# Performance work log

Hardware: AMD Instinct MI355X
Metric: run time of the kernel (lower is better)

## Reference

```python
import jax, jax.numpy as jnp
import numpy as np

N = 100000   # num nodes
E = 1200000  # num edges
D = 64       # feature dim (input and both hidden layers)
R = 4        # num relations


def setup_inputs() -> dict:
    key = jax.random.key(0)
    ks = jax.random.split(key, 16)

    def p(k, shape, scale=0.05):
        return jax.random.normal(k, shape, dtype=jnp.float32) * scale

    inp = {
        "x": p(ks[0], (N, D), 1.0),
        "src": jax.random.randint(ks[1], (E,), 0, N),
        "dst": jax.random.randint(ks[2], (E,), 0, N),
        "rel": jax.random.randint(ks[3], (E,), 0, R),
    }
    i = 4
    for layer in (1, 2):
        inp[f"conv{layer}_w"] = p(ks[i], (D, R * D)); i += 1
        inp[f"conv{layer}_b"] = jnp.zeros((D,), jnp.float32)
        inp[f"conv{layer}_ws"] = p(ks[i], (D, D)); i += 1
        inp[f"conv{layer}_bs"] = jnp.zeros((D,), jnp.float32)
        inp[f"hw{layer}_pw"] = p(ks[i], (D, 2 * D)); i += 1
        inp[f"hw{layer}_pb"] = jnp.zeros((D,), jnp.float32)
        inp[f"hw{layer}_tw"] = p(ks[i], (D, 2 * D)); i += 1
        inp[f"hw{layer}_tb"] = jnp.full((D,), -2.0, jnp.float32)  # transform bias init -2
    return inp


def _rgc(x, src, dst, rel, w, b, ws, bs):
    # RelationalGraphConv: per-(node, relation) scatter-mean of source features,
    # then linear over concatenated relation slots + self-loop linear + sigmoid.
    msg = x[src]                                  # [E, D] gather
    seg = dst * R + rel                           # [E] flattened (node, relation) id
    s = jax.ops.segment_sum(msg, seg, num_segments=N * R)          # [N*R, D]
    cnt = jax.ops.segment_sum(jnp.ones((msg.shape[0], 1), msg.dtype), seg,
                              num_segments=N * R)                  # [N*R, 1]
    upd = (s / jnp.maximum(cnt, 1.0)).reshape(N, R * x.shape[1])   # [N, R*D]
    out = upd @ w.T + b + x @ ws.T + bs
    return jax.nn.sigmoid(out)


def _highway(h, prev, pw, pb, tw, tb):
    c = jnp.concatenate([h, prev], axis=1)        # [N, 2D]
    pr = jax.nn.relu(c @ pw.T + pb)
    g = jax.nn.sigmoid(c @ tw.T + tb)
    return g * pr + (1.0 - g) * h


def reference(x, src, dst, rel,
              conv1_w, conv1_b, conv1_ws, conv1_bs,
              hw1_pw, hw1_pb, hw1_tw, hw1_tb,
              conv2_w, conv2_b, conv2_ws, conv2_bs,
              hw2_pw, hw2_pb, hw2_tw, hw2_tb):
    h1 = _rgc(x, src, dst, rel, conv1_w, conv1_b, conv1_ws, conv1_bs)
    g1 = _highway(h1, x, hw1_pw, hw1_pb, hw1_tw, hw1_tb)   # prev_gcn = input
    h2 = _rgc(g1, src, dst, rel, conv2_w, conv2_b, conv2_ws, conv2_bs)
    g2 = _highway(h2, h1, hw2_pw, hw2_pb, hw2_tw, hw2_tb)  # prev_gcn = h1 (conv1 output)
    return g2  # node_feature, [N, D]
```

## Files before the change

### kernel.cpp

```cpp
#include <hip/hip_runtime.h>

#define NN 100000
#define NE 1200000
#define NRR 400000
#define NBIN 98
#define SSZ2 384

typedef float f32x4 __attribute__((ext_vector_type(4)));
typedef __bf16 bf16x8 __attribute__((ext_vector_type(8)));

__device__ __forceinline__ float sigmoidf_(float x){ return 1.0f/(1.0f+__expf(-x)); }

__global__ __launch_bounds__(256)
void binhist_kernel(const int* __restrict__ dst, const int* __restrict__ rel,
                    int* __restrict__ bincnt){
  __shared__ int h[NBIN];
  int t = threadIdx.x;
  if (t < NBIN) h[t] = 0;
  __syncthreads();
  for (int e = blockIdx.x*256 + t; e < NE; e += 64*256){
    int bin = (dst[e]*4 + rel[e]) >> 12;
    atomicAdd(&h[bin], 1);
  }
  __syncthreads();
  if (t < NBIN && h[t]) atomicAdd(&bincnt[t], h[t]);
}

__global__ void binscan_kernel(const int* __restrict__ bincnt, int* __restrict__ binoff,
                               int* __restrict__ bincur, int* __restrict__ soff){
  if (threadIdx.x == 0){
    int s = 0;
    for (int i = 0; i < NBIN; ++i){ binoff[i] = s; bincur[i] = s; s += bincnt[i]; }
    binoff[NBIN] = NE;
    soff[NRR] = NE;
  }
}

__global__ __launch_bounds__(256)
void passA_kernel(const int* __restrict__ src, const int* __restrict__ dst,
                  const int* __restrict__ rel, int* __restrict__ bincur,
                  unsigned* __restrict__ ebin){
  __shared__ int h[NBIN], runbase[NBIN];
  int t = threadIdx.x;
  if (t < NBIN) h[t] = 0;
  __syncthreads();
  int lo = blockIdx.x*8192, hi = min(lo + 8192, NE);
  for (int e = lo + t; e < hi; e += 256)
    atomicAdd(&h[(dst[e]*4 + rel[e]) >> 12], 1);
  __syncthreads();
  if (t < NBIN){
    runbase[t] = h[t] ? atomicAdd(&bincur[t], h[t]) : 0;
    h[t] = 0;
  }
  __syncthreads();
  for (int e = lo + t; e < hi; e += 256){
    int seg = dst[e]*4 + rel[e];
    int bin = seg >> 12;
    int p = runbase[bin] + atomicAdd(&h[bin], 1);
    ebin[p] = (unsigned)src[e] | ((unsigned)(seg & 4095) << 17);
  }
}

__global__ __launch_bounds__(1024)
void passB_kernel(const unsigned* __restrict__ ebin, const int* __restrict__ binoff,
                  int* __restrict__ soff, unsigned* __restrict__ ebuck){
  __shared__ int st[4096];
  __shared__ int wsum[16], wbase[16];
  const int bin = blockIdx.x;
  const int t = threadIdx.x;
  const int base = binoff[bin], end = binoff[bin+1];
  #pragma unroll
  for (int i = 0; i < 4; ++i) st[t*4 + i] = 0;
  __syncthreads();
  for (int e = base + t; e < end; e += 1024)
    atomicAdd(&st[(ebin[e] >> 17) & 4095], 1);
  __syncthreads();
  int h0 = st[t*4], h1 = st[t*4+1], h2 = st[t*4+2], h3 = st[t*4+3];
  int lsum = h0 + h1 + h2 + h3;
  int lane = t & 63, wv = t >> 6;
  int inc = lsum;
  #pragma unroll
  for (int o = 1; o < 64; o <<= 1){ int u = __shfl_up(inc, o); if (lane >= o) inc += u; }
  if (lane == 63) wsum[wv] = inc;
  __syncthreads();
  if (t == 0){ int s = 0; for (int i = 0; i < 16; ++i){ wbase[i] = s; s += wsum[i]; } }
  __syncthreads();
  int ex = base + wbase[wv] + (inc - lsum);
  int s0 = ex, s1 = ex + h0, s2 = s1 + h1, s3 = s2 + h2;
  st[t*4] = s0; st[t*4+1] = s1; st[t*4+2] = s2; st[t*4+3] = s3;
  int sg = bin*4096 + t*4;
  if (sg   < NRR) soff[sg]   = s0;
  if (sg+1 < NRR) soff[sg+1] = s1;
  if (sg+2 < NRR) soff[sg+2] = s2;
  if (sg+3 < NRR) soff[sg+3] = s3;
  __syncthreads();
  for (int e = base + t; e < end; e += 1024){
    unsigned u = ebin[e];
    int p = atomicAdd(&st[(u >> 17) & 4095], 1);
    ebuck[p] = u & 0x1FFFFu;
  }
}

__global__ void tobf16_kernel(const float* __restrict__ xf, __bf16* __restrict__ xb){
  int i = (blockIdx.x*256 + threadIdx.x)*8;
  if (i < NN*64){
    f32x4 a = *(const f32x4*)(xf + i);
    f32x4 b = *(const f32x4*)(xf + i + 4);
    bf16x8 r;
    r[0]=(__bf16)a[0]; r[1]=(__bf16)a[1]; r[2]=(__bf16)a[2]; r[3]=(__bf16)a[3];
    r[4]=(__bf16)b[0]; r[5]=(__bf16)b[1]; r[6]=(__bf16)b[2]; r[7]=(__bf16)b[3];
    *(bf16x8*)(xb + i) = r;
  }
}

__global__ void prep_kernel(const float* __restrict__ w,  const float* __restrict__ b,
                            const float* __restrict__ ws, const float* __restrict__ bs,
                            const float* __restrict__ pw, const float* __restrict__ pb,
                            const float* __restrict__ tw, const float* __restrict__ tb,
                            __bf16* __restrict__ W1, __bf16* __restrict__ W2,
                            float* __restrict__ bias1, float* __restrict__ bias2){
  int i = blockIdx.x*256 + threadIdx.x;
  if (i < 64*320) {
    int e = i & 7, lane = (i >> 3) & 63, j = (i >> 9) & 3, kbi = i >> 11;
    int n = j*16 + (lane & 15);
    int k = kbi*32 + (lane >> 4)*8 + e;
    float v = (k < 256) ? w[n*256 + k] : ws[n*64 + (k - 256)];
    W1[i] = (__bf16)v;
  }
  if (i < 128*128) {
    int e = i & 7, lane = (i >> 3) & 63, j = (i >> 9) & 7, kbi = i >> 12;
    int n = j*16 + (lane & 15);
    int k = kbi*32 + (lane >> 4)*8 + e;
    float v = (n < 64) ? pw[n*128 + k] : tw[(n - 64)*128 + k];
    W2[i] = (__bf16)v;
  }
  if (i < 64)  bias1[i] = b[i] + bs[i];
  if (i < 128) bias2[i] = (i < 64) ? pb[i] : tb[i-64];
}

__global__ __launch_bounds__(256)
void gather_kernel(const unsigned* __restrict__ ebuck, const int* __restrict__ soff,
                   const __bf16* __restrict__ inb, __bf16* __restrict__ segb){
  __shared__ int sof[33];
  __shared__ int ssrc[SSZ2];
  const int b = blockIdx.x;
  const int t = threadIdx.x;
  if (t < 33) sof[t] = soff[b*32 + t];
  __syncthreads();
  const int e0 = sof[0], e1 = sof[32];
  for (int e = e0 + t; e < e1; e += 256){
    int o = e - e0;
    if (o < SSZ2) ssrc[o] = (int)ebuck[e];
  }
  __syncthreads();

  const int fl = t & 7;
  const int g  = t >> 3;
  int o0 = sof[g] - e0;
  int c  = sof[g+1] - sof[g];
  if (o0 + c > SSZ2) c = max(0, SSZ2 - o0);

  f32x4 a0 = {0.f,0.f,0.f,0.f}, a1 = {0.f,0.f,0.f,0.f};
  f32x4 b0 = {0.f,0.f,0.f,0.f}, b1 = {0.f,0.f,0.f,0.f};
  int i = 0;
  for (; i + 2 <= c; i += 2){
    int s0 = ssrc[o0+i], s1 = ssrc[o0+i+1];
    bf16x8 v0 = *(const bf16x8*)(&inb[(size_t)s0*64 + fl*8]);
    bf16x8 v1 = *(const bf16x8*)(&inb[(size_t)s1*64 + fl*8]);
    a0[0]+=(float)v0[0]; a0[1]+=(float)v0[1]; a0[2]+=(float)v0[2]; a0[3]+=(float)v0[3];
    a1[0]+=(float)v0[4]; a1[1]+=(float)v0[5]; a1[2]+=(float)v0[6]; a1[3]+=(float)v0[7];
    b0[0]+=(float)v1[0]; b0[1]+=(float)v1[1]; b0[2]+=(float)v1[2]; b0[3]+=(float)v1[3];
    b1[0]+=(float)v1[4]; b1[1]+=(float)v1[5]; b1[2]+=(float)v1[6]; b1[3]+=(float)v1[7];
  }
  if (i < c){
    int s0 = ssrc[o0+i];
    bf16x8 v0 = *(const bf16x8*)(&inb[(size_t)s0*64 + fl*8]);
    a0[0]+=(float)v0[0]; a0[1]+=(float)v0[1]; a0[2]+=(float)v0[2]; a0[3]+=(float)v0[3];
    a1[0]+=(float)v0[4]; a1[1]+=(float)v0[5]; a1[2]+=(float)v0[6]; a1[3]+=(float)v0[7];
  }
  float inv = 1.0f / fmaxf((float)c, 1.0f);
  bf16x8 r;
  r[0]=(__bf16)((a0[0]+b0[0])*inv); r[1]=(__bf16)((a0[1]+b0[1])*inv);
  r[2]=(__bf16)((a0[2]+b0[2])*inv); r[3]=(__bf16)((a0[3]+b0[3])*inv);
  r[4]=(__bf16)((a1[0]+b1[0])*inv); r[5]=(__bf16)((a1[1]+b1[1])*inv);
  r[6]=(__bf16)((a1[2]+b1[2])*inv); r[7]=(__bf16)((a1[3]+b1[3])*inv);

  const int sgg = b*32 + g;
  const int n   = sgg >> 2, rr = sgg & 3;
  const int nb  = n >> 4,  ml = n & 15;
  const int kbi = rr*2 + (fl >> 2);
  const int kgs = fl & 3;
  *(bf16x8*)(&segb[(size_t)((nb*8 + kbi)*64 + kgs*16 + ml)*8]) = r;
}

#define HSP 72

template<bool LAYER1>
__global__ __launch_bounds__(256, 4)
void dense_kernel(const __bf16* __restrict__ segbs,
                  const __bf16* __restrict__ xinb,
                  const __bf16* __restrict__ prevb,
                  const __bf16* __restrict__ W1s,
                  const __bf16* __restrict__ W2s,
                  const float* __restrict__ bias1,
                  const float* __restrict__ bias2,
                  __bf16* __restrict__ hb,
                  __bf16* __restrict__ gb,
                  float* __restrict__ outp)
{
  __shared__ __align__(16) __bf16 hs[64*HSP];
  __shared__ __align__(16) float outs[64*64];

  const int tid  = threadIdx.x;
  const int lane = tid & 63;
  const int wv   = tid >> 6;
  const int mloc = lane & 15;
  const int kg   = lane >> 4;
  const int wb   = blockIdx.x*64 + wv*16;
  const int arow = min(wb + mloc, NN-1);
  const int nbq  = min(wb, NN-16) >> 4;
  const size_t abase = (size_t)nbq * (8*512);

  f32x4 acc1[4] = {};

  #pragma unroll
  for (int kbi = 0; kbi < 8; ++kbi) {
    bf16x8 af = *(const bf16x8*)(&segbs[abase + (size_t)(kbi*64 + lane)*8]);
    #pragma unroll
    for (int j = 0; j < 4; ++j) {
      bf16x8 bf = *(const bf16x8*)(&W1s[((kbi*4 + j)*64 + lane)*8]);
      acc1[j] = __builtin_amdgcn_mfma_f32_16x16x32_bf16(af, bf, acc1[j], 0,0,0);
    }
  }
  #pragma unroll
  for (int kb = 0; kb < 64; kb += 32) {
    bf16x8 af = *(const bf16x8*)(&xinb[(size_t)arow*64 + kb + kg*8]);
    const int kbi = 8 + (kb >> 5);
    #pragma unroll
    for (int j = 0; j < 4; ++j) {
      bf16x8 bf = *(const bf16x8*)(&W1s[((kbi*4 + j)*64 + lane)*8]);
      acc1[j] = __builtin_amdgcn_mfma_f32_16x16x32_bf16(af, bf, acc1[j], 0,0,0);
    }
  }

  #pragma unroll
  for (int j = 0; j < 4; ++j) {
    int col = j*16 + mloc;
    float b1 = bias1[col];
    #pragma unroll
    for (int r = 0; r < 4; ++r) {
      float hv = sigmoidf_(acc1[j][r] + b1);
      acc1[j][r] = hv;
      hs[(wv*16 + kg*4 + r)*HSP + col] = (__bf16)hv;
    }
  }

  if (LAYER1) {
    #pragma unroll
    for (int i = 0; i < 2; ++i) {
      int r2 = i*8 + (lane >> 3);
      int c2 = lane & 7;
      bf16x8 v = *(const bf16x8*)(&hs[(wv*16 + r2)*HSP + c2*8]);
      int grow = wb + r2;
      if (grow < NN) *(bf16x8*)(&hb[(size_t)grow*64 + c2*8]) = v;
    }
  }

  f32x4 acc2[8] = {};
  #pragma unroll
  for (int kb = 0; kb < 64; kb += 32) {
    bf16x8 af = *(const bf16x8*)(&hs[(wv*16 + mloc)*HSP + kb + kg*8]);
    const int kbi = kb >> 5;
    #pragma unroll
    for (int j = 0; j < 8; ++j) {
      bf16x8 bf = *(const bf16x8*)(&W2s[((kbi*8 + j)*64 + lane)*8]);
      acc2[j] = __builtin_amdgcn_mfma_f32_16x16x32_bf16(af, bf, acc2[j], 0,0,0);
    }
  }
  #pragma unroll
  for (int kb = 0; kb < 64; kb += 32) {
    bf16x8 af = *(const bf16x8*)(&prevb[(size_t)arow*64 + kb + kg*8]);
    const int kbi = 2 + (kb >> 5);
    #pragma unroll
    for (int j = 0; j < 8; ++j) {
      bf16x8 bf = *(const bf16x8*)(&W2s[((kbi*8 + j)*64 + lane)*8]);
      acc2[j] = __builtin_amdgcn_mfma_f32_16x16x32_bf16(af, bf, acc2[j], 0,0,0);
    }
  }

  #pragma unroll
  for (int j = 0; j < 4; ++j) {
    int col = j*16 + mloc;
    float bp = bias2[col];
    float bt = bias2[64 + col];
    #pragma unroll
    for (int r = 0; r < 4; ++r) {
      float pr = fmaxf(acc2[j][r] + bp, 0.0f);
      float g  = sigmoidf_(acc2[j+4][r] + bt);
      float hv = acc1[j][r];
      float ov = g*pr + (1.0f - g)*hv;
      if (LAYER1) {
        hs[(wv*16 + kg*4 + r)*HSP + col] = (__bf16)ov;
      } else {
        outs[(wv*16 + kg*4 + r)*64 + col] = ov;
      }
    }
  }
  if (LAYER1) {
    #pragma unroll
    for (int i = 0; i < 2; ++i) {
      int r2 = i*8 + (lane >> 3);
      int c2 = lane & 7;
      bf16x8 v = *(const bf16x8*)(&hs[(wv*16 + r2)*HSP + c2*8]);
      int grow = wb + r2;
      if (grow < NN) *(bf16x8*)(&gb[(size_t)grow*64 + c2*8]) = v;
    }
  } else {
    #pragma unroll
    for (int i = 0; i < 4; ++i) {
      int pos = i*256 + lane*4;
      int r2 = pos >> 6, c2 = pos & 63;
      int grow = wb + r2;
      if (grow < NN)
        *(f32x4*)(&outp[(size_t)grow*64 + c2]) =
            *(const f32x4*)(&outs[(wv*16 + r2)*64 + c2]);
    }
  }
}

extern "C" void kernel_launch(void* const* d_in, const int* in_sizes, int n_in,
                              void* d_out, int out_size, void* d_ws, size_t ws_size,
                              hipStream_t stream){
  const float* x    = (const float*)d_in[0];
  const int*   src  = (const int*)d_in[1];
  const int*   dst  = (const int*)d_in[2];
  const int*   rel  = (const int*)d_in[3];
  const float* c1w  = (const float*)d_in[4];
  const float* c1b  = (const float*)d_in[5];
  const float* c1ws = (const float*)d_in[6];
  const float* c1bs = (const float*)d_in[7];
  const float* h1pw = (const float*)d_in[8];
  const float* h1pb = (const float*)d_in[9];
  const float* h1tw = (const float*)d_in[10];
  const float* h1tb = (const float*)d_in[11];
  const float* c2w  = (const float*)d_in[12];
  const float* c2b  = (const float*)d_in[13];
  const float* c2ws = (const float*)d_in[14];
  const float* c2bs = (const float*)d_in[15];
  const float* h2pw = (const float*)d_in[16];
  const float* h2pb = (const float*)d_in[17];
  const float* h2tw = (const float*)d_in[18];
  const float* h2tb = (const float*)d_in[19];

  char* p = (char*)d_ws;
  __bf16* segb = (__bf16*)p;  p += (size_t)NRR*64*2;
  __bf16* xb   = (__bf16*)p;  p += (size_t)NN*64*2;
  __bf16* h1b  = (__bf16*)p;  p += (size_t)NN*64*2;
  __bf16* g1b  = (__bf16*)p;  p += (size_t)NN*64*2;
  unsigned* ebuck = (unsigned*)p; p += (size_t)NE*4;
  unsigned* ebin  = (unsigned*)p; p += (size_t)NE*4;
  int* soff    = (int*)p;     p += (size_t)(NRR+8)*4;
  int* bincnt  = (int*)p;     p += 128*4;
  int* binoff  = (int*)p;     p += 128*4;
  int* bincur  = (int*)p;     p += 128*4;
  __bf16* W1a  = (__bf16*)p;  p += 64*320*2;
  __bf16* W2a  = (__bf16*)p;  p += 128*128*2;
  __bf16* W1b  = (__bf16*)p;  p += 64*320*2;
  __bf16* W2b  = (__bf16*)p;  p += 128*128*2;
  float* B1a   = (float*)p;   p += 64*4;
  float* B2a   = (float*)p;   p += 128*4;
  float* B1b   = (float*)p;   p += 64*4;
  float* B2b   = (float*)p;   p += 128*4;

  float* out = (float*)d_out;

  hipMemsetAsync(bincnt, 0, 128*4, stream);
  binhist_kernel<<<64, 256, 0, stream>>>(dst, rel, bincnt);
  binscan_kernel<<<1, 64, 0, stream>>>(bincnt, binoff, bincur, soff);
  passA_kernel<<<(NE+8191)/8192, 256, 0, stream>>>(src, dst, rel, bincur, ebin);
  passB_kernel<<<NBIN, 1024, 0, stream>>>(ebin, binoff, soff, ebuck);

  tobf16_kernel<<<(NN*64/8 + 255)/256, 256, 0, stream>>>(x, xb);
  prep_kernel<<<80, 256, 0, stream>>>(c1w, c1b, c1ws, c1bs, h1pw, h1pb, h1tw, h1tb,
                                      W1a, W2a, B1a, B2a);
  prep_kernel<<<80, 256, 0, stream>>>(c2w, c2b, c2ws, c2bs, h2pw, h2pb, h2tw, h2tb,
                                      W1b, W2b, B1b, B2b);

  gather_kernel<<<NRR/32, 256, 0, stream>>>(ebuck, soff, xb, segb);
  dense_kernel<true><<<(NN+63)/64, 256, 0, stream>>>(segb, xb, xb, W1a, W2a, B1a, B2a,
                                                     h1b, g1b, nullptr);
  gather_kernel<<<NRR/32, 256, 0, stream>>>(ebuck, soff, g1b, segb);
  dense_kernel<false><<<(NN+63)/64, 256, 0, stream>>>(segb, g1b, h1b, W1b, W2b, B1b, B2b,
                                                      nullptr, nullptr, out);
}
```

Before: 321.2 us.

## Widen histogram grids, merge weight prep launches, drop LDS staging in gather

Raises the binhist grid from 64 to 512 blocks and halves passA's edges per block, so the preprocessing kernels expose more parallelism. Merges the two per-layer weight-prep launches into one kernel that packs both layers. The gather kernel no longer stages source indices in shared memory; each 8-thread group reads its segment offsets and source indices straight from global memory. This also removes the 384-edge cap per block that silently truncated large segments. It saves syncthreads and launch overhead at the cost of redundant, uncoalesced index loads across the 8 lanes of each group.

```diff
diff --git a/kernel.cpp b/kernel.cpp
--- a/kernel.cpp
+++ b/kernel.cpp
@@ -4,7 +4,7 @@
 #define NE 1200000
 #define NRR 400000
 #define NBIN 98
-#define SSZ2 384
+#define EPB 4096
 
 typedef float f32x4 __attribute__((ext_vector_type(4)));
 typedef __bf16 bf16x8 __attribute__((ext_vector_type(8)));
@@ -18,7 +18,7 @@
   int t = threadIdx.x;
   if (t < NBIN) h[t] = 0;
   __syncthreads();
-  for (int e = blockIdx.x*256 + t; e < NE; e += 64*256){
+  for (int e = blockIdx.x*256 + t; e < NE; e += 512*256){
     int bin = (dst[e]*4 + rel[e]) >> 12;
     atomicAdd(&h[bin], 1);
   }
@@ -44,7 +44,7 @@
   int t = threadIdx.x;
   if (t < NBIN) h[t] = 0;
   __syncthreads();
-  int lo = blockIdx.x*8192, hi = min(lo + 8192, NE);
+  int lo = blockIdx.x*EPB, hi = min(lo + EPB, NE);
   for (int e = lo + t; e < hi; e += 256)
     atomicAdd(&h[(dst[e]*4 + rel[e]) >> 12], 1);
   __syncthreads();
@@ -117,54 +117,53 @@
                             const float* __restrict__ ws, const float* __restrict__ bs,
                             const float* __restrict__ pw, const float* __restrict__ pb,
                             const float* __restrict__ tw, const float* __restrict__ tb,
-                            __bf16* __restrict__ W1, __bf16* __restrict__ W2,
-                            float* __restrict__ bias1, float* __restrict__ bias2){
+                            const float* __restrict__ w2,  const float* __restrict__ b2,
+                            const float* __restrict__ ws2, const float* __restrict__ bs2,
+                            const float* __restrict__ pw2, const float* __restrict__ pb2,
+                            const float* __restrict__ tw2, const float* __restrict__ tb2,
+                            __bf16* __restrict__ W1a, __bf16* __restrict__ W2a,
+                            float* __restrict__ B1a, float* __restrict__ B2a,
+                            __bf16* __restrict__ W1b, __bf16* __restrict__ W2b,
+                            float* __restrict__ B1b, float* __restrict__ B2b){
   int i = blockIdx.x*256 + threadIdx.x;
   if (i < 64*320) {
     int e = i & 7, lane = (i >> 3) & 63, j = (i >> 9) & 3, kbi = i >> 11;
     int n = j*16 + (lane & 15);
     int k = kbi*32 + (lane >> 4)*8 + e;
-    float v = (k < 256) ? w[n*256 + k] : ws[n*64 + (k - 256)];
-    W1[i] = (__bf16)v;
+    float va = (k < 256) ? w[n*256 + k]  : ws[n*64 + (k - 256)];
+    float vb = (k < 256) ? w2[n*256 + k] : ws2[n*64 + (k - 256)];
+    W1a[i] = (__bf16)va;
+    W1b[i] = (__bf16)vb;
   }
   if (i < 128*128) {
     int e = i & 7, lane = (i >> 3) & 63, j = (i >> 9) & 7, kbi = i >> 12;
     int n = j*16 + (lane & 15);
     int k = kbi*32 + (lane >> 4)*8 + e;
-    float v = (n < 64) ? pw[n*128 + k] : tw[(n - 64)*128 + k];
-    W2[i] = (__bf16)v;
-  }
-  if (i < 64)  bias1[i] = b[i] + bs[i];
-  if (i < 128) bias2[i] = (i < 64) ? pb[i] : tb[i-64];
+    float va = (n < 64) ? pw[n*128 + k]  : tw[(n - 64)*128 + k];
+    float vb = (n < 64) ? pw2[n*128 + k] : tw2[(n - 64)*128 + k];
+    W2a[i] = (__bf16)va;
+    W2b[i] = (__bf16)vb;
+  }
+  if (i < 64)  { B1a[i] = b[i] + bs[i];  B1b[i] = b2[i] + bs2[i]; }
+  if (i < 128) { B2a[i] = (i < 64) ? pb[i] : tb[i-64];
+                 B2b[i] = (i < 64) ? pb2[i] : tb2[i-64]; }
 }
 
 __global__ __launch_bounds__(256)
 void gather_kernel(const unsigned* __restrict__ ebuck, const int* __restrict__ soff,
                    const __bf16* __restrict__ inb, __bf16* __restrict__ segb){
-  __shared__ int sof[33];
-  __shared__ int ssrc[SSZ2];
-  const int b = blockIdx.x;
-  const int t = threadIdx.x;
-  if (t < 33) sof[t] = soff[b*32 + t];
-  __syncthreads();
-  const int e0 = sof[0], e1 = sof[32];
-  for (int e = e0 + t; e < e1; e += 256){
-    int o = e - e0;
-    if (o < SSZ2) ssrc[o] = (int)ebuck[e];
-  }
-  __syncthreads();
-
-  const int fl = t & 7;
-  const int g  = t >> 3;
-  int o0 = sof[g] - e0;
-  int c  = sof[g+1] - sof[g];
-  if (o0 + c > SSZ2) c = max(0, SSZ2 - o0);
+  const int sgg = blockIdx.x*32 + (threadIdx.x >> 3);
+  const int fl  = threadIdx.x & 7;
+  const int e0 = soff[sgg];
+  const int e1 = soff[sgg + 1];
+  const int c  = e1 - e0;
 
   f32x4 a0 = {0.f,0.f,0.f,0.f}, a1 = {0.f,0.f,0.f,0.f};
   f32x4 b0 = {0.f,0.f,0.f,0.f}, b1 = {0.f,0.f,0.f,0.f};
   int i = 0;
   for (; i + 2 <= c; i += 2){
-    int s0 = ssrc[o0+i], s1 = ssrc[o0+i+1];
+    int s0 = (int)ebuck[e0 + i];
+    int s1 = (int)ebuck[e0 + i + 1];
     bf16x8 v0 = *(const bf16x8*)(&inb[(size_t)s0*64 + fl*8]);
     bf16x8 v1 = *(const bf16x8*)(&inb[(size_t)s1*64 + fl*8]);
     a0[0]+=(float)v0[0]; a0[1]+=(float)v0[1]; a0[2]+=(float)v0[2]; a0[3]+=(float)v0[3];
@@ -173,7 +172,7 @@
     b1[0]+=(float)v1[4]; b1[1]+=(float)v1[5]; b1[2]+=(float)v1[6]; b1[3]+=(float)v1[7];
   }
   if (i < c){
-    int s0 = ssrc[o0+i];
+    int s0 = (int)ebuck[e0 + i];
     bf16x8 v0 = *(const bf16x8*)(&inb[(size_t)s0*64 + fl*8]);
     a0[0]+=(float)v0[0]; a0[1]+=(float)v0[1]; a0[2]+=(float)v0[2]; a0[3]+=(float)v0[3];
     a1[0]+=(float)v0[4]; a1[1]+=(float)v0[5]; a1[2]+=(float)v0[6]; a1[3]+=(float)v0[7];
@@ -185,7 +184,6 @@
   r[4]=(__bf16)((a1[0]+b1[0])*inv); r[5]=(__bf16)((a1[1]+b1[1])*inv);
   r[6]=(__bf16)((a1[2]+b1[2])*inv); r[7]=(__bf16)((a1[3]+b1[3])*inv);
 
-  const int sgg = b*32 + g;
   const int n   = sgg >> 2, rr = sgg & 3;
   const int nb  = n >> 4,  ml = n & 15;
   const int kbi = rr*2 + (fl >> 2);
@@ -375,16 +373,15 @@
   float* out = (float*)d_out;
 
   hipMemsetAsync(bincnt, 0, 128*4, stream);
-  binhist_kernel<<<64, 256, 0, stream>>>(dst, rel, bincnt);
+  binhist_kernel<<<512, 256, 0, stream>>>(dst, rel, bincnt);
   binscan_kernel<<<1, 64, 0, stream>>>(bincnt, binoff, bincur, soff);
-  passA_kernel<<<(NE+8191)/8192, 256, 0, stream>>>(src, dst, rel, bincur, ebin);
+  passA_kernel<<<(NE+EPB-1)/EPB, 256, 0, stream>>>(src, dst, rel, bincur, ebin);
   passB_kernel<<<NBIN, 1024, 0, stream>>>(ebin, binoff, soff, ebuck);
 
   tobf16_kernel<<<(NN*64/8 + 255)/256, 256, 0, stream>>>(x, xb);
   prep_kernel<<<80, 256, 0, stream>>>(c1w, c1b, c1ws, c1bs, h1pw, h1pb, h1tw, h1tb,
-                                      W1a, W2a, B1a, B2a);
-  prep_kernel<<<80, 256, 0, stream>>>(c2w, c2b, c2ws, c2bs, h2pw, h2pb, h2tw, h2tb,
-                                      W1b, W2b, B1b, B2b);
+                                      c2w, c2b, c2ws, c2bs, h2pw, h2pb, h2tw, h2tb,
+                                      W1a, W2a, B1a, B2a, W1b, W2b, B1b, B2b);
 
   gather_kernel<<<NRR/32, 256, 0, stream>>>(ebuck, soff, xb, segb);
   dense_kernel<true><<<(NN+63)/64, 256, 0, stream>>>(segb, xb, xb, W1a, W2a, B1a, B2a,
```

Measured after the change: 298.4 us, median of 3. 1.08x faster.
